# Optimization experiments

Hardware: AMD Instinct MI355X
Metric: run time of the kernel (lower is better)

Reference implementation:

```python
import jax, jax.numpy as jnp
import numpy as np

MU = 0.75
H = W = 256


def _bending_energy_one(pred):
    """pred: (2, 256, 256) probabilities. Returns scalar bending energy."""
    mask = (pred[1] > 0.5).astype(jnp.float32)  # (H, W) binary nucleus mask
    p = jnp.pad(mask, 1)
    # 8-neighbor count (3x3 ones kernel with zero center)
    nc = (p[:-2, :-2] + p[:-2, 1:-1] + p[:-2, 2:] +
          p[1:-1, :-2] + p[1:-1, 2:] +
          p[2:, :-2] + p[2:, 1:-1] + p[2:, 2:])
    contour = (mask == 1.0) & (nc < 8.0)  # (H, W) bool
    flat = contour.reshape(-1)            # (H*W,)
    N = flat.shape[0]
    # Stable argsort puts contour pixel indices first, in ascending
    # (row-major) order == torch.nonzero ordering. Fixed output shape.
    order = jnp.argsort(~flat, stable=True)  # (N,) int
    m = flat.sum()                            # number of contour points
    rows = (order // W).astype(jnp.float32)
    cols = (order % W).astype(jnp.float32)
    pts = jnp.stack([rows, cols], axis=-1)    # (N, 2)

    v1 = pts[1:-1] - pts[:-2]   # point - prev_point, centers 1..N-2
    v2 = pts[2:] - pts[1:-1]    # next_point - point
    cross = v1[:, 0] * v2[:, 1] - v1[:, 1] * v2[:, 0]
    dot = (v1 * v2).sum(-1)
    n1 = jnp.sqrt((v1 ** 2).sum(-1))
    n2 = jnp.sqrt((v2 ** 2).sum(-1))
    curv = jnp.where(cross == 0.0, 0.0,
                     2.0 * jnp.abs(cross) / (n1 * n2 + dot))
    delta = jnp.where(cross >= 0.0, 0.0, 1.0)
    be = (1.0 - delta + delta * MU) * curv ** 2 / (n1 + n2)
    # valid centers are indices 1..m-2 of the contour list -> j <= m-3
    j = jnp.arange(N - 2)
    valid = j <= (m - 3)
    return jnp.where(valid, be, 0.0).sum()


def setup_inputs() -> dict:
    key = jax.random.key(0)
    k1, k2 = jax.random.split(key)
    B = 128
    inp = jax.random.normal(k1, (B, 2, H, W), dtype=jnp.float32)
    tgt = jax.random.uniform(k2, (B, 2, H, W), dtype=jnp.float32)
    return {"input": inp, "target": tgt}


def reference(input, target):
    per_image = jax.vmap(_bending_energy_one)(target)  # (B,)
    return per_image.sum() / input.shape[0]
```

## Files before the change

kernel.cpp:

```cpp
#include <hip/hip_runtime.h>

typedef unsigned long long ull;
#define NW 1024

__global__ __launch_bounds__(1024)
void contour_build_kernel(const float* __restrict__ target,
                          ull* __restrict__ cwg,
                          float* __restrict__ out) {
    __shared__ ull lb[34 * 4];

    const int img  = blockIdx.x;
    const int band = blockIdx.y;
    const int tid  = threadIdx.x;
    const int wave = tid >> 6, lane = tid & 63;

    if (img == 0 && band == 0 && tid == 0) out[0] = 0.0f;

    const float* imgp = target + (size_t)img * 131072 + 65536;
    const int r0 = band * 32 - 1;

    for (int wr = wave; wr < 34; wr += 16) {
        const int gr = r0 + wr;
        const bool inb = (gr >= 0 && gr <= 255);
        const float* rowp = imgp + ((size_t)(inb ? gr : 0) << 8);
        float v0 = inb ? rowp[lane]       : 0.0f;
        float v1 = inb ? rowp[64 + lane]  : 0.0f;
        float v2 = inb ? rowp[128 + lane] : 0.0f;
        float v3 = inb ? rowp[192 + lane] : 0.0f;
        ull b0 = __ballot(v0 > 0.5f);
        ull b1 = __ballot(v1 > 0.5f);
        ull b2 = __ballot(v2 > 0.5f);
        ull b3 = __ballot(v3 > 0.5f);
        if (lane == 0) {
            lb[wr * 4 + 0] = b0; lb[wr * 4 + 1] = b1;
            lb[wr * 4 + 2] = b2; lb[wr * 4 + 3] = b3;
        }
    }
    __syncthreads();

    if (tid < 128) {
        const int k  = tid;
        const int lr = 1 + (k >> 2);
        const int wp = k & 3;
        auto get = [&](int rr, int ww) -> ull {
            return (ww < 0 || ww > 3) ? 0ULL : lb[(rr << 2) + ww];
        };
        ull A  = get(lr - 1, wp);
        ull C  = lb[(lr << 2) + wp];
        ull Bx = get(lr + 1, wp);
        ull Ap = get(lr - 1, wp - 1), An = get(lr - 1, wp + 1);
        ull Cp = get(lr,     wp - 1), Cn = get(lr,     wp + 1);
        ull Bp = get(lr + 1, wp - 1), Bn = get(lr + 1, wp + 1);
        ull interior =
            ((A  << 1) | (Ap >> 63)) & A  & ((A  >> 1) | (An << 63)) &
            ((C  << 1) | (Cp >> 63)) &      ((C  >> 1) | (Cn << 63)) &
            ((Bx << 1) | (Bp >> 63)) & Bx & ((Bx >> 1) | (Bn << 63));
        cwg[(size_t)img * NW + band * 128 + k] = C & ~interior;
    }
}

__global__ __launch_bounds__(1024)
void energy_kernel(const ull* __restrict__ cwg,
                   float* __restrict__ out, float inv_b) {
#pragma clang fp contract(off)
    __shared__ unsigned short idx[65536];
    __shared__ int   wsums[16];
    __shared__ float fsum[16];

    const int img  = blockIdx.x;
    const int tid  = threadIdx.x;
    const int wave = tid >> 6, lane = tid & 63;

    ull w = cwg[(size_t)img * NW + tid];
    const int pc = __popcll(w);

    int c = pc;
    for (int d = 1; d < 64; d <<= 1) {
        int t = __shfl_up(c, d);
        if (lane >= d) c += t;
    }
    if (lane == 63) wsums[wave] = c;
    __syncthreads();
    if (wave == 0 && lane < 16) {
        int s = wsums[lane];
        for (int d = 1; d < 16; d <<= 1) {
            int t = __shfl_up(s, d, 16);
            if (lane >= d) s += t;
        }
        wsums[lane] = s;
    }
    __syncthreads();

    int pos = c - pc + (wave > 0 ? wsums[wave - 1] : 0);
    const int base = tid << 6;
    while (w) {
        int b = __builtin_ctzll(w);
        w &= w - 1;
        idx[pos++] = (unsigned short)(base + b);
    }
    const int m = wsums[15];
    __syncthreads();

    float sum = 0.0f;
    for (int j = tid; j < m - 2; j += 1024) {
        const int p0 = idx[j], p1 = idx[j + 1], p2 = idx[j + 2];
        float r0f = (float)(p0 >> 8), c0f = (float)(p0 & 255);
        float r1f = (float)(p1 >> 8), c1f = (float)(p1 & 255);
        float r2f = (float)(p2 >> 8), c2f = (float)(p2 & 255);
        float v1r = r1f - r0f, v1c = c1f - c0f;
        float v2r = r2f - r1f, v2c = c2f - c1f;
        float cross = v1r * v2c - v1c * v2r;
        if (cross != 0.0f) {
            float dot = v1r * v2r + v1c * v2c;
            float n1 = sqrtf(v1r * v1r + v1c * v1c);
            float n2 = sqrtf(v2r * v2r + v2c * v2c);
            float curv = (2.0f * fabsf(cross)) / (n1 * n2 + dot);
            float factor = (cross >= 0.0f) ? 1.0f : 0.75f;
            sum += (factor * (curv * curv)) / (n1 + n2);
        }
    }

    for (int off = 32; off > 0; off >>= 1) sum += __shfl_down(sum, off);
    if (lane == 0) fsum[wave] = sum;
    __syncthreads();
    if (tid == 0) {
        float t = 0.0f;
        for (int i = 0; i < 16; ++i) t += fsum[i];
        atomicAdd(out, t * inv_b);
    }
}

extern "C" void kernel_launch(void* const* d_in, const int* in_sizes, int n_in,
                              void* d_out, int out_size, void* d_ws, size_t ws_size,
                              hipStream_t stream) {
    const float* target = (const float*)d_in[1];
    float* out = (float*)d_out;
    const int B = in_sizes[1] / (2 * 256 * 256);
    ull* cwg = (ull*)d_ws;

    contour_build_kernel<<<dim3(B, 8), dim3(1024), 0, stream>>>(target, cwg, out);
    energy_kernel<<<dim3(B), dim3(1024), 0, stream>>>(cwg, out, 1.0f / (float)B);
}
```

Measured before the change: 150.6 us.

## Move contour stencil into energy kernel; make first kernel a pure ballot pass

```diff
diff --git a/kernel.cpp b/kernel.cpp
--- a/kernel.cpp
+++ b/kernel.cpp
@@ -3,66 +3,30 @@
 typedef unsigned long long ull;
 #define NW 1024
 
-__global__ __launch_bounds__(1024)
-void contour_build_kernel(const float* __restrict__ target,
-                          ull* __restrict__ cwg,
-                          float* __restrict__ out) {
-    __shared__ ull lb[34 * 4];
+__global__ __launch_bounds__(512)
+void ballot_kernel(const float* __restrict__ target,
+                   ull* __restrict__ mbg,
+                   float* __restrict__ out) {
+    const int lane = threadIdx.x & 63;
+    const int gw = blockIdx.x * 8 + (threadIdx.x >> 6);
 
-    const int img  = blockIdx.x;
-    const int band = blockIdx.y;
-    const int tid  = threadIdx.x;
-    const int wave = tid >> 6, lane = tid & 63;
+    if (gw == 0 && lane == 0) out[0] = 0.0f;
 
-    if (img == 0 && band == 0 && tid == 0) out[0] = 0.0f;
-
-    const float* imgp = target + (size_t)img * 131072 + 65536;
-    const int r0 = band * 32 - 1;
-
-    for (int wr = wave; wr < 34; wr += 16) {
-        const int gr = r0 + wr;
-        const bool inb = (gr >= 0 && gr <= 255);
-        const float* rowp = imgp + ((size_t)(inb ? gr : 0) << 8);
-        float v0 = inb ? rowp[lane]       : 0.0f;
-        float v1 = inb ? rowp[64 + lane]  : 0.0f;
-        float v2 = inb ? rowp[128 + lane] : 0.0f;
-        float v3 = inb ? rowp[192 + lane] : 0.0f;
-        ull b0 = __ballot(v0 > 0.5f);
-        ull b1 = __ballot(v1 > 0.5f);
-        ull b2 = __ballot(v2 > 0.5f);
-        ull b3 = __ballot(v3 > 0.5f);
-        if (lane == 0) {
-            lb[wr * 4 + 0] = b0; lb[wr * 4 + 1] = b1;
-            lb[wr * 4 + 2] = b2; lb[wr * 4 + 3] = b3;
-        }
-    }
-    __syncthreads();
-
-    if (tid < 128) {
-        const int k  = tid;
-        const int lr = 1 + (k >> 2);
-        const int wp = k & 3;
-        auto get = [&](int rr, int ww) -> ull {
-            return (ww < 0 || ww > 3) ? 0ULL : lb[(rr << 2) + ww];
-        };
-        ull A  = get(lr - 1, wp);
-        ull C  = lb[(lr << 2) + wp];
-        ull Bx = get(lr + 1, wp);
-        ull Ap = get(lr - 1, wp - 1), An = get(lr - 1, wp + 1);
-        ull Cp = get(lr,     wp - 1), Cn = get(lr,     wp + 1);
-        ull Bp = get(lr + 1, wp - 1), Bn = get(lr + 1, wp + 1);
-        ull interior =
-            ((A  << 1) | (Ap >> 63)) & A  & ((A  >> 1) | (An << 63)) &
-            ((C  << 1) | (Cp >> 63)) &      ((C  >> 1) | (Cn << 63)) &
-            ((Bx << 1) | (Bp >> 63)) & Bx & ((Bx >> 1) | (Bn << 63));
-        cwg[(size_t)img * NW + band * 128 + k] = C & ~interior;
+    #pragma unroll 4
+    for (int i = 0; i < 16; ++i) {
+        const int w = gw + i * 8192;
+        const int img = w >> 10, k = w & 1023;
+        float v = target[(size_t)img * 131072 + 65536 + (k << 6) + lane];
+        ull b = __ballot(v > 0.5f);
+        if (lane == 0) mbg[w] = b;
     }
 }
 
 __global__ __launch_bounds__(1024)
-void energy_kernel(const ull* __restrict__ cwg,
+void energy_kernel(const ull* __restrict__ mbg,
                    float* __restrict__ out, float inv_b) {
 #pragma clang fp contract(off)
+    __shared__ ull mask[NW];
     __shared__ unsigned short idx[65536];
     __shared__ int   wsums[16];
     __shared__ float fsum[16];
@@ -71,9 +35,30 @@
     const int tid  = threadIdx.x;
     const int wave = tid >> 6, lane = tid & 63;
 
-    ull w = cwg[(size_t)img * NW + tid];
+    mask[tid] = mbg[(size_t)img * NW + tid];
+    __syncthreads();
+
+    ull w;
+    {
+        const int r = tid >> 2, wp = tid & 3;
+        auto get = [&](int rr, int ww) -> ull {
+            return (rr < 0 || rr > 255 || ww < 0 || ww > 3)
+                       ? 0ULL : mask[(rr << 2) + ww];
+        };
+        ull A  = get(r - 1, wp);
+        ull C  = mask[tid];
+        ull Bx = get(r + 1, wp);
+        ull Ap = get(r - 1, wp - 1), An = get(r - 1, wp + 1);
+        ull Cp = get(r,     wp - 1), Cn = get(r,     wp + 1);
+        ull Bp = get(r + 1, wp - 1), Bn = get(r + 1, wp + 1);
+        ull interior =
+            ((A  << 1) | (Ap >> 63)) & A  & ((A  >> 1) | (An << 63)) &
+            ((C  << 1) | (Cp >> 63)) &      ((C  >> 1) | (Cn << 63)) &
+            ((Bx << 1) | (Bp >> 63)) & Bx & ((Bx >> 1) | (Bn << 63));
+        w = C & ~interior;
+    }
+
     const int pc = __popcll(w);
-
     int c = pc;
     for (int d = 1; d < 64; d <<= 1) {
         int t = __shfl_up(c, d);
@@ -136,8 +121,8 @@
     const float* target = (const float*)d_in[1];
     float* out = (float*)d_out;
     const int B = in_sizes[1] / (2 * 256 * 256);
-    ull* cwg = (ull*)d_ws;
+    ull* mbg = (ull*)d_ws;
 
-    contour_build_kernel<<<dim3(B, 8), dim3(1024), 0, stream>>>(target, cwg, out);
-    energy_kernel<<<dim3(B), dim3(1024), 0, stream>>>(cwg, out, 1.0f / (float)B);
+    ballot_kernel<<<dim3(B * 8), dim3(512), 0, stream>>>(target, mbg, out);
+    energy_kernel<<<dim3(B), dim3(1024), 0, stream>>>(mbg, out, 1.0f / (float)B);
 }
```

New measurement: 148.3 us. No clear change (-1.5%).
